# Optimization experiments

Hardware: AMD Instinct MI355X
Metric: run time of the kernel (lower is better)

Reference implementation:

```python
import jax, jax.numpy as jnp
import numpy as np

B, N, D, K = 4, 8192, 128, 16


def setup_inputs() -> dict:
    key = jax.random.key(0)
    ks = jax.random.split(key, 12)
    w = lambda k, s: (jax.random.normal(k, s, jnp.float32) * 0.02)
    return {
        "xyz": jax.random.normal(ks[0], (B, N, 3), jnp.float32),
        "feat": jax.random.normal(ks[1], (B, N, D), jnp.float32),
        # Linear weights stored as (in, out); apply as x @ W + b
        "Wq": w(ks[2], (D, D)), "bq": jnp.zeros((D,), jnp.float32),
        "Wk": w(ks[3], (D, D)), "bk": jnp.zeros((D,), jnp.float32),
        "Wv": w(ks[4], (D, D)), "bv": jnp.zeros((D,), jnp.float32),
        "Wp1": w(ks[5], (3, D)), "bp1": jnp.zeros((D,), jnp.float32),
        "Wp2": w(ks[6], (D, D)), "bp2": jnp.zeros((D,), jnp.float32),
        "Wo": w(ks[7], (D, D)), "bo": jnp.zeros((D,), jnp.float32),
        "gamma": jnp.float32(0.5),
    }


def reference(xyz, feat, Wq, bq, Wk, bk, Wv, bv, Wp1, bp1, Wp2, bp2, Wo, bo, gamma):
    # pairwise squared distance (B,N,N)
    sq = jnp.sum(xyz * xyz, axis=-1)
    dist = sq[:, :, None] + sq[:, None, :] - 2.0 * jnp.einsum("bnc,bmc->bnm", xyz, xyz)
    # K nearest neighbors (smallest distance)
    _, idx = jax.lax.top_k(-dist, K)  # (B,N,K)
    bidx = jnp.arange(B)[:, None, None]
    n_xyz = xyz[bidx, idx]    # (B,N,K,3)
    n_feat = feat[bidx, idx]  # (B,N,K,D)

    q = (feat @ Wq + bq)[:, :, None, :]    # (B,N,1,D)
    kk = n_feat @ Wk + bk                  # (B,N,K,D)
    v = n_feat @ Wv + bv                   # (B,N,K,D)

    rel_pos = xyz[:, :, None, :] - n_xyz   # (B,N,K,3)
    pos_enc = jax.nn.relu(rel_pos @ Wp1 + bp1) @ Wp2 + bp2  # (B,N,K,D)

    # per-channel-summed attention score, softmax over neighbor axis
    score = jnp.sum(q - kk + pos_enc, axis=-1, keepdims=True)  # (B,N,K,1)
    attn = jax.nn.softmax(score, axis=-2)

    agg = jnp.sum(attn * (v + pos_enc), axis=2)  # (B,N,D)
    out = agg @ Wo + bo
    return feat + gamma * out
```

## Files before the change

### kernel.cpp

```cpp
#include <hip/hip_runtime.h>
#include <hip/hip_bf16.h>

#define BATCH 4
#define NPTS  8192
#define DIM   128
#define KNN   16
#define NROWS (BATCH * NPTS)

#define SPLITS 16
#define RANGE  512
#define TILE   256
#define LWIN   512
#define NWIN   4

using u64  = unsigned long long;
using u32  = unsigned int;

__device__ __forceinline__ unsigned short f2bf(float f) {
    u32 u = __float_as_uint(f);
    u32 r = (u + 0x7FFFu + ((u >> 16) & 1u)) >> 16;
    return (unsigned short)r;
}
__device__ __forceinline__ u32 fordkey(float f) {
    u32 u = __float_as_uint(f);
    return (u & 0x80000000u) ? ~u : (u | 0x80000000u);
}
__device__ __forceinline__ float invkey(u32 k) {
    u32 u = (k & 0x80000000u) ? (k & 0x7FFFFFFFu) : ~k;
    return __uint_as_float(u);
}

__device__ __forceinline__ void insert16u(u32 key, u32* ks) {
    if (key < ks[15]) {
#pragma unroll
        for (int t = 0; t < 16; ++t) {
            u32 lo = key < ks[t] ? key : ks[t];
            u32 hi = key < ks[t] ? ks[t] : key;
            ks[t] = lo;
            key = hi;
        }
    }
}

__device__ __forceinline__ float pdist(float4 me, float4 c) {
    float dot = __fadd_rn(__fadd_rn(__fmul_rn(me.x, c.x), __fmul_rn(me.y, c.y)),
                          __fmul_rn(me.z, c.z));
    return __fsub_rn(__fadd_rn(me.w, c.w), __fmul_rn(2.0f, dot));
}

__global__ __launch_bounds__(256) void prep_weights(const float* __restrict__ Wk,
                                                    const float* __restrict__ Wp2,
                                                    float* __restrict__ wk,
                                                    float* __restrict__ w2) {
    int tid = threadIdx.x;
    int c = tid & 127;
    const float* src = (tid < 128) ? Wk : Wp2;
    float s = 0.f;
    for (int d = 0; d < DIM; ++d) s += src[c * DIM + d];
    if (tid < 128) wk[c] = s;
    else           w2[c] = s;
}

__global__ __launch_bounds__(256) void conv_weights(const float* __restrict__ Wv,
                                                    const float* __restrict__ Wp2,
                                                    const float* __restrict__ Wo,
                                                    u32* __restrict__ Wb) {
    int i = blockIdx.x * 256 + threadIdx.x;
    int which = i >> 13, off = i & 8191;
    const float* W = (which == 0) ? Wv : (which == 1 ? Wp2 : Wo);
    float2 w = ((const float2*)W)[off];
    Wb[i] = (u32)f2bf(w.x) | ((u32)f2bf(w.y) << 16);
}

__global__ __launch_bounds__(256) void prep_points(const float* __restrict__ xyz,
                                                   const float* __restrict__ feat,
                                                   const float* __restrict__ wk,
                                                   float4* __restrict__ pts,
                                                   float* __restrict__ sK) {
    int lid = threadIdx.x & 63;
    int p = blockIdx.x * 4 + (threadIdx.x >> 6);
    float f_lo = feat[(size_t)p * DIM + lid];
    float f_hi = feat[(size_t)p * DIM + 64 + lid];
    float s = fmaf(f_lo, wk[lid], f_hi * wk[64 + lid]);
#pragma unroll
    for (int m = 32; m >= 1; m >>= 1) s += __shfl_xor(s, m);
    if (lid == 0) {
        float x = xyz[p * 3 + 0];
        float y = xyz[p * 3 + 1];
        float z = xyz[p * 3 + 2];
        float sq = __fadd_rn(__fadd_rn(__fmul_rn(x, x), __fmul_rn(y, y)), __fmul_rn(z, z));
        pts[p] = make_float4(x, y, z, sq);
        sK[p] = s;
    }
}

__global__ __launch_bounds__(256) void knn_limpass(const float4* __restrict__ pts,
                                                   float* __restrict__ dl16q) {
    __shared__ float4 tile[256];
    int y = blockIdx.y;
    int wavein = threadIdx.x >> 6, lane = threadIdx.x & 63;
    int q = blockIdx.x * 256 + wavein * 64 + lane;
    int b = blockIdx.x >> 5;
    float4 me = pts[q];

    float c0[4], c1[4], c2[4], c3[4];
#pragma unroll
    for (int t = 0; t < 4; ++t) { c0[t] = INFINITY; c1[t] = INFINITY;
                                  c2[t] = INFINITY; c3[t] = INFINITY; }
    float lim = INFINITY;
    float A = -INFINITY;

#define INS4(CH, DV)                                                          \
    if ((DV) < CH[3]) {                                                       \
        float dd_ = (DV);                                                     \
        _Pragma("unroll")                                                     \
        for (int t_ = 0; t_ < 4; ++t_) {                                      \
            float lo_ = fminf(dd_, CH[t_]);                                   \
            float hi_ = fmaxf(dd_, CH[t_]);                                   \
            CH[t_] = lo_; dd_ = hi_;                                          \
        }                                                                     \
    }

    for (int tb = 0; tb < LWIN / 256; ++tb) {
        __syncthreads();
        {
            float4 c = pts[b * NPTS + y * LWIN + tb * 256 + threadIdx.x];
            tile[threadIdx.x] = make_float4(c.x, c.y, c.z, -0.5f * c.w);
        }
        __syncthreads();

        int cstart = 0;
        if (tb == 0) {
#pragma unroll
            for (int jj = 0; jj < 32; ++jj) {
                float4 c = tile[jj];
                float s = fmaf(me.x, c.x, fmaf(me.y, c.y, fmaf(me.z, c.z, c.w)));
                float d = fmaf(-2.0f, s, me.w);
                if ((jj & 3) == 0)      { INS4(c0, d); }
                else if ((jj & 3) == 1) { INS4(c1, d); }
                else if ((jj & 3) == 2) { INS4(c2, d); }
                else                    { INS4(c3, d); }
            }
            lim = fmaxf(fmaxf(c0[3], c1[3]), fmaxf(c2[3], c3[3]));
            A = 0.5f * (me.w - lim);
            cstart = 32;
        }
        for (int cw = cstart; cw < 256; cw += 32) {
            u32 mask = 0;
#pragma unroll
            for (int jj = 0; jj < 32; ++jj) {
                float4 c = tile[cw + jj];
                float s = fmaf(me.x, c.x, fmaf(me.y, c.y, fmaf(me.z, c.z, c.w)));
                mask = (mask << 1) | (u32)(s >= A);
            }
#define POP_INS(CH)                                                           \
            if (mask) {                                                       \
                int pos_ = __builtin_ctz(mask); mask &= mask - 1;             \
                int jj_ = cw + 31 - pos_;                                     \
                float4 c_ = tile[jj_];                                        \
                float s_ = fmaf(me.x, c_.x,                                   \
                            fmaf(me.y, c_.y, fmaf(me.z, c_.z, c_.w)));        \
                float d_ = fmaf(-2.0f, s_, me.w);                             \
                INS4(CH, d_);                                                 \
            }
            while (mask) {
                POP_INS(c0);
                POP_INS(c1);
                POP_INS(c2);
                POP_INS(c3);
            }
#undef POP_INS
            lim = fmaxf(fmaxf(c0[3], c1[3]), fmaxf(c2[3], c3[3]));
            A = 0.5f * (me.w - lim);
        }
    }
#undef INS4
    float4* dst = (float4*)(dl16q + (size_t)q * 64 + y * 16);
    dst[0] = make_float4(c0[0], c0[1], c0[2], c0[3]);
    dst[1] = make_float4(c1[0], c1[1], c1[2], c1[3]);
    dst[2] = make_float4(c2[0], c2[1], c2[2], c2[3]);
    dst[3] = make_float4(c3[0], c3[1], c3[2], c3[3]);
}

__global__ __launch_bounds__(256) void bound_merge(const float* __restrict__ dl16q,
                                                   float* __restrict__ Tq) {
    int wavein = threadIdx.x >> 6, lane = threadIdx.x & 63;
    int q = blockIdx.x * 4 + wavein;
    float v = dl16q[(size_t)q * 64 + lane];
    float got = v;
#pragma unroll
    for (int it = 0; it < 16; ++it) {
        float m = v;
#pragma unroll
        for (int s = 32; s >= 1; s >>= 1) m = fminf(m, __shfl_xor(m, s));
        if (v == m) v = INFINITY;
        got = m;
    }
    if (lane == 0) Tq[q] = got;
}

__global__ __launch_bounds__(256) void knn_partial(const float4* __restrict__ pts,
                                                   const float* __restrict__ Tq,
                                                   unsigned short* __restrict__ part16) {
    __shared__ float4 tile[TILE];
    int r = blockIdx.y;
    int wavein = threadIdx.x >> 6, lane = threadIdx.x & 63;
    int q = blockIdx.x * 256 + wavein * 64 + lane;
    int b = blockIdx.x >> 5;
    float4 me = pts[q];

    float gate_d = Tq[q] + 2.0e-4f;
    u32 kk[16];
#pragma unroll
    for (int t = 0; t < 16; ++t) kk[t] = 0xFFFFFFFFu;
    float A = 0.5f * (me.w - gate_d) - 1.0e-4f;

    for (int tb = 0; tb < RANGE / TILE; ++tb) {
        __syncthreads();
        int jb = r * RANGE + tb * TILE;
        {
            float4 c = pts[b * NPTS + jb + threadIdx.x];
            tile[threadIdx.x] = make_float4(c.x, c.y, c.z, -0.5f * c.w);
        }
        __syncthreads();

        u32 m[8];
#pragma unroll
        for (int w = 0; w < 8; ++w) {
            u32 mask = 0;
#pragma unroll
            for (int jj = 0; jj < 32; ++jj) {
                float4 c = tile[w * 32 + jj];
                float s = fmaf(me.x, c.x, fmaf(me.y, c.y, fmaf(me.z, c.z, c.w)));
                mask = (mask << 1) | (u32)(s >= A);
            }
            m[w] = mask;
        }
        int cnt = __popc(m[0]) + __popc(m[1]) + __popc(m[2]) + __popc(m[3]) +
                  __popc(m[4]) + __popc(m[5]) + __popc(m[6]) + __popc(m[7]);

        u32 cur = m[0];
        int w = 0;
        for (int i = 0; i < cnt; ++i) {
            while (cur == 0) {
                ++w;
                cur = (w == 1) ? m[1] : (w == 2) ? m[2] : (w == 3) ? m[3] :
                      (w == 4) ? m[4] : (w == 5) ? m[5] : (w == 6) ? m[6] : m[7];
            }
            int pos = __builtin_ctz(cur);
            cur &= cur - 1;
            int jj = (w << 5) + (31 - pos);
            float4 c = tile[jj];
            float s = fmaf(me.x, c.x, fmaf(me.y, c.y, fmaf(me.z, c.z, c.w)));
            float dt = fmaf(-2.0f, s, me.w);
            u32 key = (fordkey(dt) & 0xFFFFE000u) | (u32)(jb + jj);
            insert16u(key, kk);
        }
        float nl = invkey((kk[15] & 0xFFFFE000u) | 0x1FFFu) + 1.0e-4f;
        gate_d = (nl < gate_d) ? nl : gate_d;
        A = 0.5f * (me.w - gate_d) - 1.0e-4f;
    }
    u32* dst = (u32*)(part16 + (size_t)q * 256 + r * 16);
#pragma unroll
    for (int t = 0; t < 8; ++t) {
        u32 a = kk[2 * t], c = kk[2 * t + 1];
        u32 i0 = (a == 0xFFFFFFFFu) ? 0xFFFFu : (a & 0x1FFFu);
        u32 i1 = (c == 0xFFFFFFFFu) ? 0xFFFFu : (c & 0x1FFFu);
        dst[t] = i0 | (i1 << 16);
    }
}

__global__ __launch_bounds__(256) void knn_merge(const float4* __restrict__ pts,
                                                 const unsigned short* __restrict__ part16,
                                                 int* __restrict__ idx16) {
    int wavein = threadIdx.x >> 6, lane = threadIdx.x & 63;
    int q = blockIdx.x * 4 + wavein;
    int b = q >> 13;
    float4 me = pts[q];
    ushort4 e = *(const ushort4*)(part16 + (size_t)q * 256 + lane * 4);
    u64 k0, k1, k2, k3;
    {
        u32 id, ida;
        id = e.x; ida = (id != 0xFFFFu) ? id : 0u;
        k0 = (id != 0xFFFFu) ? (((u64)fordkey(pdist(me, pts[b * NPTS + ida])) << 32) | id) : ~0ull;
        id = e.y; ida = (id != 0xFFFFu) ? id : 0u;
        k1 = (id != 0xFFFFu) ? (((u64)fordkey(pdist(me, pts[b * NPTS + ida])) << 32) | id) : ~0ull;
        id = e.z; ida = (id != 0xFFFFu) ? id : 0u;
        k2 = (id != 0xFFFFu) ? (((u64)fordkey(pdist(me, pts[b * NPTS + ida])) << 32) | id) : ~0ull;
        id = e.w; ida = (id != 0xFFFFu) ? id : 0u;
        k3 = (id != 0xFFFFu) ? (((u64)fordkey(pdist(me, pts[b * NPTS + ida])) << 32) | id) : ~0ull;
    }
    u64 t;
    if (k1 < k0) { t = k0; k0 = k1; k1 = t; }
    if (k3 < k2) { t = k2; k2 = k3; k3 = t; }
    if (k2 < k0) { t = k0; k0 = k2; k2 = t; }
    if (k3 < k1) { t = k1; k1 = k3; k3 = t; }
    if (k2 < k1) { t = k1; k1 = k2; k2 = t; }

    u32 curh = (u32)(k0 >> 32), curl = (u32)k0;
    int head = 0;
    u32 gotl = 0;
#pragma unroll
    for (int it = 0; it < 16; ++it) {
        u32 mh = curh;
#pragma unroll
        for (int s = 32; s >= 1; s >>= 1) {
            u32 o = __shfl_xor(mh, s);
            mh = (o < mh) ? o : mh;
        }
        u64 bal = __ballot(curh == mh);
        u32 wlo;
        if (__builtin_popcountll(bal) == 1) {
            int wl = __builtin_ctzll(bal);
            wlo = __shfl(curl, wl);
        } else {
            u32 cand = (curh == mh) ? curl : 0xFFFFFFFFu;
#pragma unroll
            for (int s = 32; s >= 1; s >>= 1) {
                u32 o = __shfl_xor(cand, s);
                cand = (o < cand) ? o : cand;
            }
            wlo = cand;
        }
        if (curh == mh && curl == wlo) {
            head++;
            u64 nx = (head == 1) ? k1 : (head == 2) ? k2 : (head == 3) ? k3 : ~0ull;
            curh = (u32)(nx >> 32);
            curl = (u32)nx;
        }
        if (lane == it) gotl = wlo;
    }
    if (lane < 16) idx16[q * KNN + lane] = (int)gotl;
}

template <int MODE>
__global__ __launch_bounds__(256) void gemm32(const float* __restrict__ X,
                                              const u32* __restrict__ Wb,
                                              const float* __restrict__ bias,
                                              const float* __restrict__ add,
                                              const float* __restrict__ featb,
                                              const float* __restrict__ gammap,
                                              float* __restrict__ outv) {
    __shared__ u32 Ws[DIM * DIM / 2];
    __shared__ float Xs[8 * DIM];
    __shared__ float bs[DIM];
    int tid = threadIdx.x;
    {
        const uint4* src = (const uint4*)Wb;
        uint4* dst = (uint4*)Ws;
        for (int i = tid; i < DIM * DIM / 8; i += 256) dst[i] = src[i];
    }
    if (tid < 128) bs[tid] = bias[tid];
    float gamma = 0.f;
    if (MODE == 2) gamma = *gammap;

    int rowBase = blockIdx.x * 32;
    int d4 = (tid & 31) * 4;
    int row = tid >> 5;

    for (int it = 0; it < 4; ++it) {
        int r0 = rowBase + it * 8;
        __syncthreads();
        ((float4*)Xs)[tid] = ((const float4*)(X + (size_t)r0 * DIM))[tid];
        __syncthreads();

        float a0 = bs[d4], a1 = bs[d4 + 1], a2 = bs[d4 + 2], a3 = bs[d4 + 3];
        const float* xr = &Xs[row * DIM];
#pragma unroll 8
        for (int c = 0; c < DIM; ++c) {
            float x = xr[c];
            uint2 w = *(const uint2*)&Ws[c * (DIM / 2) + (d4 >> 1)];
            a0 = fmaf(x, __uint_as_float(w.x << 16), a0);
            a1 = fmaf(x, __uint_as_float(w.x & 0xFFFF0000u), a1);
            a2 = fmaf(x, __uint_as_float(w.y << 16), a2);
            a3 = fmaf(x, __uint_as_float(w.y & 0xFFFF0000u), a3);
        }
        size_t off = (size_t)(r0 + row) * DIM + d4;
        if (MODE == 1) {
            float4 ad = *(const float4*)(add + off);
            a0 += ad.x; a1 += ad.y; a2 += ad.z; a3 += ad.w;
        }
        if (MODE == 2) {
            float4 fb = *(const float4*)(featb + off);
            a0 = fmaf(gamma, a0, fb.x);
            a1 = fmaf(gamma, a1, fb.y);
            a2 = fmaf(gamma, a2, fb.z);
            a3 = fmaf(gamma, a3, fb.w);
        }
        *(float4*)(outv + off) = make_float4(a0, a1, a2, a3);
    }
}

__global__ __launch_bounds__(256, 5) void stage_c(const float4* __restrict__ pts,
                                               const int* __restrict__ idx16,
                                               const float* __restrict__ sK,
                                               const float* __restrict__ w2,
                                               const float* __restrict__ Wp1,
                                               const float* __restrict__ bp1,
                                               const float* __restrict__ Vf,
                                               float* __restrict__ vagg,
                                               float* __restrict__ hbar) {
    int wavein = threadIdx.x >> 6;
    int lid = threadIdx.x & 63;
    int p = blockIdx.x * 4 + wavein;
    int b = p >> 13;
    float4 me = pts[p];

    float wx_lo = Wp1[lid],        wx_hi = Wp1[64 + lid];
    float wy_lo = Wp1[128 + lid],  wy_hi = Wp1[192 + lid];
    float wz_lo = Wp1[256 + lid],  wz_hi = Wp1[320 + lid];
    float bl    = bp1[lid],        bh    = bp1[64 + lid];
    float w2l   = w2[lid],         w2h   = w2[64 + lid];

    int myidx = idx16[p * KNN + (lid & 15)];
    float h_lo[KNN], h_hi[KNN];
    float sc = -INFINITY;

#pragma unroll
    for (int k = 0; k < KNN; ++k) {
        int j = __shfl(myidx, k);
        int g = b * NPTS + j;
        float4 nb = pts[g];
        float rx = me.x - nb.x, ry = me.y - nb.y, rz = me.z - nb.z;
        float hl = fmaxf(0.f, fmaf(rx, wx_lo, fmaf(ry, wy_lo, fmaf(rz, wz_lo, bl))));
        float hh = fmaxf(0.f, fmaf(rx, wx_hi, fmaf(ry, wy_hi, fmaf(rz, wz_hi, bh))));
        h_lo[k] = hl;
        h_hi[k] = hh;
        float s = fmaf(hl, w2l, hh * w2h);
#pragma unroll
        for (int m = 32; m >= 1; m >>= 1) s += __shfl_xor(s, m);
        float score = s - sK[g];
        if (lid == k) sc = score;
    }
    float mx = sc;
#pragma unroll
    for (int m = 8; m >= 1; m >>= 1) mx = fmaxf(mx, __shfl_xor(mx, m));
    float e = (lid < 16) ? __expf(sc - mx) : 0.f;
    float ssum = e;
#pragma unroll
    for (int m = 8; m >= 1; m >>= 1) ssum += __shfl_xor(ssum, m);
    float a = e / ssum;

    float acc_lo = 0.f, acc_hi = 0.f, hb_lo = 0.f, hb_hi = 0.f;
#pragma unroll
    for (int k = 0; k < KNN; ++k) {
        float ak = __shfl(a, k);
        int j = __shfl(myidx, k);
        size_t g = (size_t)(b * NPTS + j) * DIM;
        acc_lo = fmaf(ak, Vf[g + lid], acc_lo);
        acc_hi = fmaf(ak, Vf[g + 64 + lid], acc_hi);
        hb_lo = fmaf(ak, h_lo[k], hb_lo);
        hb_hi = fmaf(ak, h_hi[k], hb_hi);
    }
    size_t o = (size_t)p * DIM;
    vagg[o + lid] = acc_lo;
    vagg[o + 64 + lid] = acc_hi;
    hbar[o + lid] = hb_lo;
    hbar[o + 64 + lid] = hb_hi;
}

extern "C" void kernel_launch(void* const* d_in, const int* in_sizes, int n_in,
                              void* d_out, int out_size, void* d_ws, size_t ws_size,
                              hipStream_t stream) {
    const float* xyz   = (const float*)d_in[0];
    const float* feat  = (const float*)d_in[1];
    const float* Wk    = (const float*)d_in[4];
    const float* Wv    = (const float*)d_in[6];
    const float* bv    = (const float*)d_in[7];
    const float* Wp1   = (const float*)d_in[8];
    const float* bp1   = (const float*)d_in[9];
    const float* Wp2   = (const float*)d_in[10];
    const float* bp2   = (const float*)d_in[11];
    const float* Wo    = (const float*)d_in[12];
    const float* bo    = (const float*)d_in[13];
    const float* gamma = (const float*)d_in[14];
    float* out = (float*)d_out;

    char* ws = (char*)d_ws;
    const size_t KB = 1024, MB = 1024 * 1024;
    float*  wk    = (float*)(ws + 0);
    float*  w2    = (float*)(ws + 4 * KB);
    float4* pts   = (float4*)(ws + 16 * KB);
    float*  sKv   = (float*)(ws + 544 * KB);
    u32*    Wb    = (u32*)(ws + 688 * KB);
    float*  Tq    = (float*)(ws + 1 * MB);
    float*  dl16q = (float*)(ws + 5 * MB);
    unsigned short* part16 = (unsigned short*)(ws + 5 * MB);
    float*  vagg  = (float*)(ws + 5 * MB);
    float*  hbarp = (float*)(ws + 21 * MB);
    int*    idx16 = (int*)(ws + 37 * MB);
    float*  Vf    = (float*)(ws + 39 * MB);
    float*  T1    = (float*)(ws + 39 * MB);

    prep_weights<<<1, 256, 0, stream>>>(Wk, Wp2, wk, w2);
    conv_weights<<<96, 256, 0, stream>>>(Wv, Wp2, Wo, Wb);
    prep_points<<<NROWS / 4, 256, 0, stream>>>(xyz, feat, wk, pts, sKv);
    gemm32<0><<<1024, 256, 0, stream>>>(feat, Wb, bv, nullptr, nullptr, nullptr, Vf);
    knn_limpass<<<dim3(NROWS / 256, NWIN), 256, 0, stream>>>(pts, dl16q);
    bound_merge<<<NROWS / 4, 256, 0, stream>>>(dl16q, Tq);
    knn_partial<<<dim3(NROWS / 256, SPLITS), 256, 0, stream>>>(pts, Tq, part16);
    knn_merge<<<NROWS / 4, 256, 0, stream>>>(pts, part16, idx16);
    stage_c<<<NROWS / 4, 256, 0, stream>>>(pts, idx16, sKv, w2, Wp1, bp1, Vf, vagg, hbarp);
    gemm32<1><<<1024, 256, 0, stream>>>(hbarp, Wb + 8192, bp2, vagg, nullptr, nullptr, T1);
    gemm32<2><<<1024, 256, 0, stream>>>(T1, Wb + 16384, bo, nullptr, feat, gamma, out);
}
```

Before: 452.9 us.

## Rewrite knn_partial as lane-transposed ballot filter with rare overflow fallback

The candidate-filtering kernel no longer stages points through shared memory with per-thread bitmask loops and insertion sorts. Each lane now holds 8 candidates in registers, and for each of the 64 queries in the wave the query coordinates are broadcast via readlane; a ballot builds that query's 64-bit survivor mask per chunk. Survivors are written directly as indices with no sorting. Only queries with more than 16 survivors fall back to a serial scan with insertion sort. This removes LDS traffic, barriers and the divergent insertion loop, but loses the in-range gate tightening between tiles and risks divergence when overflow is common.

```diff
diff --git a/kernel.cpp b/kernel.cpp
--- a/kernel.cpp
+++ b/kernel.cpp
@@ -9,7 +9,6 @@
 
 #define SPLITS 16
 #define RANGE  512
-#define TILE   256
 #define LWIN   512
 #define NWIN   4
 
@@ -46,6 +45,10 @@
     float dot = __fadd_rn(__fadd_rn(__fmul_rn(me.x, c.x), __fmul_rn(me.y, c.y)),
                           __fmul_rn(me.z, c.z));
     return __fsub_rn(__fadd_rn(me.w, c.w), __fmul_rn(2.0f, dot));
+}
+
+__device__ __forceinline__ float rdlane(float v, int l) {
+    return __int_as_float(__builtin_amdgcn_readlane(__float_as_int(v), l));
 }
 
 __global__ __launch_bounds__(256) void prep_weights(const float* __restrict__ Wk,
@@ -202,71 +205,76 @@
 __global__ __launch_bounds__(256) void knn_partial(const float4* __restrict__ pts,
                                                    const float* __restrict__ Tq,
                                                    unsigned short* __restrict__ part16) {
-    __shared__ float4 tile[TILE];
     int r = blockIdx.y;
     int wavein = threadIdx.x >> 6, lane = threadIdx.x & 63;
     int q = blockIdx.x * 256 + wavein * 64 + lane;
     int b = blockIdx.x >> 5;
+    int jb = r * RANGE;
     float4 me = pts[q];
-
     float gate_d = Tq[q] + 2.0e-4f;
-    u32 kk[16];
-#pragma unroll
-    for (int t = 0; t < 16; ++t) kk[t] = 0xFFFFFFFFu;
     float A = 0.5f * (me.w - gate_d) - 1.0e-4f;
 
-    for (int tb = 0; tb < RANGE / TILE; ++tb) {
-        __syncthreads();
-        int jb = r * RANGE + tb * TILE;
-        {
-            float4 c = pts[b * NPTS + jb + threadIdx.x];
-            tile[threadIdx.x] = make_float4(c.x, c.y, c.z, -0.5f * c.w);
-        }
-        __syncthreads();
-
-        u32 m[8];
-#pragma unroll
-        for (int w = 0; w < 8; ++w) {
-            u32 mask = 0;
-#pragma unroll
-            for (int jj = 0; jj < 32; ++jj) {
-                float4 c = tile[w * 32 + jj];
-                float s = fmaf(me.x, c.x, fmaf(me.y, c.y, fmaf(me.z, c.z, c.w)));
-                mask = (mask << 1) | (u32)(s >= A);
+    float4 cand[8];
+#pragma unroll
+    for (int ch = 0; ch < 8; ++ch) {
+        float4 c = pts[b * NPTS + jb + ch * 64 + lane];
+        cand[ch] = make_float4(c.x, c.y, c.z, -0.5f * c.w);
+    }
+
+    u64 msk[8];
+#pragma unroll
+    for (int ch = 0; ch < 8; ++ch) msk[ch] = 0;
+
+    for (int qq = 0; qq < 64; ++qq) {
+        float mx = rdlane(me.x, qq);
+        float my = rdlane(me.y, qq);
+        float mz = rdlane(me.z, qq);
+        float Aq = rdlane(A, qq);
+        bool keep = (lane == qq);
+#pragma unroll
+        for (int ch = 0; ch < 8; ++ch) {
+            float s = fmaf(mx, cand[ch].x,
+                       fmaf(my, cand[ch].y, fmaf(mz, cand[ch].z, cand[ch].w)));
+            u64 bal = __ballot(s >= Aq);
+            msk[ch] = keep ? bal : msk[ch];
+        }
+    }
+
+    unsigned short* dst = part16 + (size_t)q * 256 + r * 16;
+    int slot = 0;
+#pragma unroll
+    for (int ch = 0; ch < 8; ++ch) {
+        u64 mm = msk[ch];
+        while (mm) {
+            int pos = __builtin_ctzll(mm);
+            mm &= mm - 1;
+            if (slot < 16) dst[slot] = (unsigned short)(jb + ch * 64 + pos);
+            ++slot;
+        }
+    }
+    bool over = (slot > 16);
+    for (int t = slot; t < 16; ++t) dst[t] = 0xFFFFu;
+
+    if (__any(over)) {
+        if (over) {
+            u32 kk[16];
+#pragma unroll
+            for (int t = 0; t < 16; ++t) kk[t] = 0xFFFFFFFFu;
+            for (int jj = 0; jj < RANGE; ++jj) {
+                float4 c = pts[b * NPTS + jb + jj];
+                float s = fmaf(me.x, c.x,
+                           fmaf(me.y, c.y, fmaf(me.z, c.z, -0.5f * c.w)));
+                if (s >= A) {
+                    float dt = fmaf(-2.0f, s, me.w);
+                    u32 key = (fordkey(dt) & 0xFFFFE000u) | (u32)(jb + jj);
+                    insert16u(key, kk);
+                }
             }
-            m[w] = mask;
-        }
-        int cnt = __popc(m[0]) + __popc(m[1]) + __popc(m[2]) + __popc(m[3]) +
-                  __popc(m[4]) + __popc(m[5]) + __popc(m[6]) + __popc(m[7]);
-
-        u32 cur = m[0];
-        int w = 0;
-        for (int i = 0; i < cnt; ++i) {
-            while (cur == 0) {
-                ++w;
-                cur = (w == 1) ? m[1] : (w == 2) ? m[2] : (w == 3) ? m[3] :
-                      (w == 4) ? m[4] : (w == 5) ? m[5] : (w == 6) ? m[6] : m[7];
-            }
-            int pos = __builtin_ctz(cur);
-            cur &= cur - 1;
-            int jj = (w << 5) + (31 - pos);
-            float4 c = tile[jj];
-            float s = fmaf(me.x, c.x, fmaf(me.y, c.y, fmaf(me.z, c.z, c.w)));
-            float dt = fmaf(-2.0f, s, me.w);
-            u32 key = (fordkey(dt) & 0xFFFFE000u) | (u32)(jb + jj);
-            insert16u(key, kk);
-        }
-        float nl = invkey((kk[15] & 0xFFFFE000u) | 0x1FFFu) + 1.0e-4f;
-        gate_d = (nl < gate_d) ? nl : gate_d;
-        A = 0.5f * (me.w - gate_d) - 1.0e-4f;
-    }
-    u32* dst = (u32*)(part16 + (size_t)q * 256 + r * 16);
-#pragma unroll
-    for (int t = 0; t < 8; ++t) {
-        u32 a = kk[2 * t], c = kk[2 * t + 1];
-        u32 i0 = (a == 0xFFFFFFFFu) ? 0xFFFFu : (a & 0x1FFFu);
-        u32 i1 = (c == 0xFFFFFFFFu) ? 0xFFFFu : (c & 0x1FFFu);
-        dst[t] = i0 | (i1 << 16);
+#pragma unroll
+            for (int t = 0; t < 16; ++t)
+                dst[t] = (kk[t] == 0xFFFFFFFFu) ? (unsigned short)0xFFFFu
+                                                : (unsigned short)(kk[t] & 0x1FFFu);
+        }
     }
 }
 
```

Measured after the change: 483.6 us. +6.8%, slower.
